# Kernel tuning notes

Hardware: AMD Instinct MI355X
Metric: run time of the kernel (lower is better)

Reference implementation:

```python
import jax, jax.numpy as jnp
import numpy as np

N = 100000      # nodes
E = 1600000     # edges (avg degree 16)
F_IN = 256      # num_features
H2 = 128        # nhid * 2 (layer 1 width)
H = 64          # nhid (layer 2 width)
C = 10          # num_classes


def setup_inputs() -> dict:
    key = jax.random.key(0)
    ks = jax.random.split(key, 8)
    x = jax.random.normal(ks[0], (N, F_IN), dtype=jnp.float32)
    edge_index = jax.random.randint(ks[1], (2, E), 0, N, dtype=jnp.int64)
    W1 = jax.random.normal(ks[2], (F_IN, H2), dtype=jnp.float32) / np.float32(np.sqrt(F_IN))
    b1 = jnp.zeros((H2,), jnp.float32)
    W2 = jax.random.normal(ks[3], (H2, H), dtype=jnp.float32) / np.float32(np.sqrt(H2))
    b2 = jnp.zeros((H,), jnp.float32)
    Wl = jax.random.normal(ks[4], (H, C), dtype=jnp.float32) / np.float32(np.sqrt(H))
    bl = jnp.zeros((C,), jnp.float32)
    return {"x": x, "edge_index": edge_index, "W1": W1, "b1": b1,
            "W2": W2, "b2": b2, "Wl": Wl, "bl": bl}


def reference(x, edge_index, W1, b1, W2, b2, Wl, bl):
    # --- GCN normalization with self-loops (PyG GCNConv default) ---
    loops = jnp.arange(N, dtype=edge_index.dtype)
    src = jnp.concatenate([edge_index[0], loops])  # message sources
    dst = jnp.concatenate([edge_index[1], loops])  # message targets
    deg = jax.ops.segment_sum(jnp.ones(src.shape[0], x.dtype), dst, num_segments=N)
    dinv = jnp.where(deg > 0, jax.lax.rsqrt(deg), 0.0)
    norm = dinv[src] * dinv[dst]                   # [E+N]

    def gcn_conv(h, W, b):
        m = h @ W                                  # transform first (out_channels small)
        agg = jax.ops.segment_sum(m[src] * norm[:, None], dst, num_segments=N)
        return agg + b

    h = jax.nn.relu(gcn_conv(x, W1, b1))           # [N, H2]
    h = jax.nn.relu(gcn_conv(h, W2, b2))           # [N, H]
    logits = h @ Wl + bl                            # [N, C]
    return jax.nn.log_softmax(logits, axis=-1)
```

## Files before the change

### kernel.cpp

```cpp
#include <hip/hip_runtime.h>


typedef unsigned short ushort_t;
typedef unsigned int uint_t;
typedef __attribute__((ext_vector_type(8))) short short8;
typedef __attribute__((ext_vector_type(4))) float floatx4;

static __device__ __forceinline__ ushort_t f2bf(float f) {
    union { float f; uint_t u; } c; c.f = f;
    return (ushort_t)((c.u + 0x8000u) >> 16);
}
static __device__ __forceinline__ float bf2f(ushort_t h) {
    union { uint_t u; float f; } c; c.u = ((uint_t)h) << 16;
    return c.f;
}
static __device__ __forceinline__ float2 up2(uint_t p) {
    union { uint_t u; float f; } lo, hi;
    lo.u = p << 16; hi.u = p & 0xffff0000u;
    return make_float2(lo.f, hi.f);
}
static __device__ __forceinline__ uint_t pk2bf(float a, float b) {
    return ((uint_t)f2bf(b) << 16) | (uint_t)f2bf(a);
}
static __device__ __forceinline__ void ld_lds16(void* lds, const void* g) {
    __builtin_amdgcn_global_load_lds(
        (const __attribute__((address_space(1))) unsigned int*)g,
        (__attribute__((address_space(3))) unsigned int*)lds, 16, 0, 0);
}

#define NBMAX 800
#define ECAP  4096

__global__ __launch_bounds__(256) void hist_kernel(
    const int* __restrict__ dst, int* __restrict__ histG,
    const float* __restrict__ W1, const float* __restrict__ W2,
    ushort_t* __restrict__ W1t, ushort_t* __restrict__ W2t,
    int* __restrict__ done, int E, int NB, int GB) {
    if ((int)blockIdx.x >= GB) {
        if ((int)blockIdx.x == GB && threadIdx.x == 0) *done = 0;
        int i = ((int)blockIdx.x - GB) * 256 + threadIdx.x;
        if (i < 256 * 128) {
            int k = i / 128, n = i % 128;
            W1t[n * 256 + k] = f2bf(W1[i]);
        }
        int j = i - 256 * 128;
        if (j >= 0 && j < 128 * 64) {
            int k = j / 64, n = j % 64;
            W2t[n * 128 + k] = f2bf(W2[j]);
        }
        return;
    }
    __shared__ int h[NBMAX];
    for (int i = threadIdx.x; i < NB; i += 256) h[i] = 0;
    __syncthreads();
    int i16 = (blockIdx.x * 256 + threadIdx.x) * 16;
    if (i16 + 15 < E) {
        #pragma unroll
        for (int u = 0; u < 4; u++) {
            int4 d = *(const int4*)(dst + i16 + u * 4);
            atomicAdd(&h[d.x >> 7], 1);
            atomicAdd(&h[d.y >> 7], 1);
            atomicAdd(&h[d.z >> 7], 1);
            atomicAdd(&h[d.w >> 7], 1);
        }
    } else {
        for (int e = i16; e < E; e++) atomicAdd(&h[dst[e] >> 7], 1);
    }
    __syncthreads();
    int* outp = histG + (size_t)blockIdx.x * NB;
    for (int i = threadIdx.x; i < NB; i += 256) outp[i] = h[i];
}

__global__ __launch_bounds__(256) void scan_bucket(
    int* __restrict__ histG, int* __restrict__ totG, int* __restrict__ bbase,
    int* __restrict__ done, int GB, int NB, int nblk) {
    __shared__ int isLast;
    __shared__ int s[256];
    int b = blockIdx.x * 256 + threadIdx.x;
    if (b < NB) {
        int run = 0;
        int g = 0;
        for (; g + 16 <= GB; g += 16) {
            int vv[16];
            #pragma unroll
            for (int u = 0; u < 16; u++) vv[u] = histG[(size_t)(g + u) * NB + b];
            #pragma unroll
            for (int u = 0; u < 16; u++) {
                histG[(size_t)(g + u) * NB + b] = run;
                run += vv[u];
            }
        }
        for (; g < GB; g++) {
            int v = histG[(size_t)g * NB + b];
            histG[(size_t)g * NB + b] = run;
            run += v;
        }
        totG[b] = run;
    }
    __threadfence();
    __syncthreads();
    if (threadIdx.x == 0)
        isLast = (atomicAdd(done, 1) == nblk - 1);
    __syncthreads();
    if (!isLast) return;
    __threadfence();
    int running = 0;
    int nch = (NB + 255) / 256;
    for (int c = 0; c < nch; c++) {
        int j = c * 256 + threadIdx.x;
        int v = (j < NB) ? totG[j] : 0;
        s[threadIdx.x] = v;
        __syncthreads();
        for (int off = 1; off < 256; off <<= 1) {
            int tmp = (threadIdx.x >= off) ? s[threadIdx.x - off] : 0;
            __syncthreads();
            s[threadIdx.x] += tmp;
            __syncthreads();
        }
        if (j < NB) bbase[j] = s[threadIdx.x] - v + running;
        int ctot = s[255];
        __syncthreads();
        running += ctot;
    }
    if (threadIdx.x == 0) bbase[NB] = running;
}

__global__ __launch_bounds__(256) void scatter_kernel(
    const int* __restrict__ src, const int* __restrict__ dst,
    const int* __restrict__ histG, const int* __restrict__ bbase,
    int* __restrict__ packed, int E, int NB) {
    __shared__ int lbase[NBMAX];
    const int* row = histG + (size_t)blockIdx.x * NB;
    for (int i = threadIdx.x; i < NB; i += 256)
        lbase[i] = bbase[i] + row[i];
    __syncthreads();
    int i16 = (blockIdx.x * 256 + threadIdx.x) * 16;
    if (i16 + 15 < E) {
        #pragma unroll
        for (int u = 0; u < 4; u++) {
            int4 s4 = *(const int4*)(src + i16 + u * 4);
            int4 d4 = *(const int4*)(dst + i16 + u * 4);
            int p;
            p = atomicAdd(&lbase[d4.x >> 7], 1); packed[p] = s4.x | ((d4.x & 127) << 17);
            p = atomicAdd(&lbase[d4.y >> 7], 1); packed[p] = s4.y | ((d4.y & 127) << 17);
            p = atomicAdd(&lbase[d4.z >> 7], 1); packed[p] = s4.z | ((d4.z & 127) << 17);
            p = atomicAdd(&lbase[d4.w >> 7], 1); packed[p] = s4.w | ((d4.w & 127) << 17);
        }
    } else {
        for (int e = i16; e < E; e++) {
            int d = dst[e];
            int p = atomicAdd(&lbase[d >> 7], 1);
            packed[p] = src[e] | ((d & 127) << 17);
        }
    }
}

__global__ __launch_bounds__(256) void bucket_csr(
    const int* __restrict__ packed, const int* __restrict__ bbase,
    int* __restrict__ rowptr, int* __restrict__ csr,
    float* __restrict__ dinv, int N, int NB) {
    __shared__ int ebuf[ECAP];
    __shared__ int cnt[128];
    __shared__ int pl[128];
    __shared__ int s[256];
    const int b = blockIdx.x;
    const int t = threadIdx.x;
    const int lo = bbase[b];
    const int hi = bbase[b + 1];
    int m = hi - lo;
    if (m > ECAP) m = ECAP;
    for (int i = t; i < m; i += 256) ebuf[i] = packed[lo + i];
    if (t < 128) cnt[t] = 0;
    __syncthreads();
    for (int i = t; i < m; i += 256) atomicAdd(&cnt[ebuf[i] >> 17], 1);
    __syncthreads();
    const int node0 = b << 7;
    int c = (t < 128) ? cnt[t] : 0;
    if (t < 128 && node0 + t < N)
        dinv[node0 + t] = rsqrtf((float)(c + 1));
    s[t] = c;
    __syncthreads();
    for (int off = 1; off < 256; off <<= 1) {
        int tmp = (t >= off) ? s[t - off] : 0;
        __syncthreads();
        s[t] += tmp;
        __syncthreads();
    }
    int excl = s[t] - c;
    if (t < 128) {
        pl[t] = excl;
        if (node0 + t <= N) rowptr[node0 + t] = lo + excl;
    }
    __syncthreads();
    for (int i = t; i < m; i += 256) {
        int e = ebuf[i];
        int p = atomicAdd(&pl[e >> 17], 1);
        csr[lo + p] = e & 0x1FFFF;
    }
}

__global__ __launch_bounds__(256) void gemm1_mfma(
    const float* __restrict__ A, const ushort_t* __restrict__ Bt,
    const float* __restrict__ dinv, ushort_t* __restrict__ out, int M) {
    __shared__ float    As[64 * 256];
    __shared__ ushort_t Bs[128 * 256];
    const int tid = threadIdx.x;
    const int l = tid & 63;
    const int wave = tid >> 6;
    const int lrow = l & 15, hh = l >> 4;
    const int m0 = blockIdx.x * 64;

    #pragma unroll
    for (int rd = 0; rd < 16; rd++) {
        int idx = rd * 256 + tid;
        int r = idx >> 6, cs = idx & 63;
        int row = m0 + r; if (row >= M) row = M - 1;
        int cl = cs ^ (r & 7);
        ld_lds16(&As[idx * 4], A + (size_t)row * 256 + cl * 4);
    }
    #pragma unroll
    for (int rd = 0; rd < 16; rd++) {
        int idx = rd * 256 + tid;
        int n = idx >> 5, cs = idx & 31;
        int cl = cs ^ (n & 7);
        ld_lds16(&Bs[idx * 8], Bt + (size_t)n * 256 + cl * 8);
    }
    __syncthreads();

    floatx4 acc[8];
    #pragma unroll
    for (int nt = 0; nt < 8; nt++)
        acc[nt] = (floatx4){0.f, 0.f, 0.f, 0.f};

    const int wr = wave * 16 + lrow;
    #pragma unroll
    for (int kk = 0; kk < 8; kk++) {
        int c0 = kk * 8 + hh * 2;
        float4 u = *(const float4*)&As[wr * 256 + ((c0    ) ^ (wr & 7)) * 4];
        float4 v = *(const float4*)&As[wr * 256 + ((c0 + 1) ^ (wr & 7)) * 4];
        short8 afr;
        afr[0] = (short)f2bf(u.x); afr[1] = (short)f2bf(u.y);
        afr[2] = (short)f2bf(u.z); afr[3] = (short)f2bf(u.w);
        afr[4] = (short)f2bf(v.x); afr[5] = (short)f2bf(v.y);
        afr[6] = (short)f2bf(v.z); afr[7] = (short)f2bf(v.w);
        short8 bfr[8];
        #pragma unroll
        for (int nt = 0; nt < 8; nt++) {
            int n = nt * 16 + lrow;
            int c = kk * 4 + hh;
            bfr[nt] = *(const short8*)&Bs[n * 256 + (c ^ (n & 7)) * 8];
        }
        #pragma unroll
        for (int nt = 0; nt < 8; nt++)
            acc[nt] = __builtin_amdgcn_mfma_f32_16x16x32_bf16(
                afr, bfr[nt], acc[nt], 0, 0, 0);
    }

    const int mbase = m0 + wave * 16 + hh * 4;
    float4 dv = *(const float4*)&dinv[mbase];
    float d[4] = {dv.x, dv.y, dv.z, dv.w};
    #pragma unroll
    for (int i = 0; i < 4; i++) {
        int m = mbase + i;
        if (m < M) {
            #pragma unroll
            for (int nt = 0; nt < 8; nt++)
                out[(size_t)m * 128 + nt * 16 + lrow] =
                    f2bf(acc[nt][i] * d[i]);
        } else if (m == M) {
            #pragma unroll
            for (int nt = 0; nt < 8; nt++)
                out[(size_t)M * 128 + nt * 16 + lrow] = 0;
        }
    }
}

__global__ __launch_bounds__(256) void gemm2_mfma(
    const ushort_t* __restrict__ A, const ushort_t* __restrict__ Bt,
    const float* __restrict__ dinv, ushort_t* __restrict__ out, int M) {
    __shared__ ushort_t As[64 * 128];
    __shared__ ushort_t Bs[64 * 128];
    const int tid = threadIdx.x;
    const int l = tid & 63;
    const int wave = tid >> 6;
    const int lrow = l & 15, hh = l >> 4;
    const int m0 = blockIdx.x * 64;

    #pragma unroll
    for (int rd = 0; rd < 4; rd++) {
        int idx = rd * 256 + tid;
        int r = idx >> 4, cs = idx & 15;
        int row = m0 + r; if (row >= M) row = M - 1;
        int cl = cs ^ (r & 7);
        ld_lds16(&As[idx * 8], A + (size_t)row * 128 + cl * 8);
    }
    #pragma unroll
    for (int rd = 0; rd < 4; rd++) {
        int idx = rd * 256 + tid;
        int n = idx >> 4, cs = idx & 15;
        int cl = cs ^ (n & 7);
        ld_lds16(&Bs[idx * 8], Bt + (size_t)n * 128 + cl * 8);
    }
    __syncthreads();

    floatx4 acc[4];
    #pragma unroll
    for (int nt = 0; nt < 4; nt++)
        acc[nt] = (floatx4){0.f, 0.f, 0.f, 0.f};

    const int wr = wave * 16 + lrow;
    #pragma unroll
    for (int kk = 0; kk < 4; kk++) {
        int c0 = kk * 4 + hh;
        short8 afr = *(const short8*)&As[wr * 128 + (c0 ^ (wr & 7)) * 8];
        short8 bfr[4];
        #pragma unroll
        for (int nt = 0; nt < 4; nt++) {
            int n = nt * 16 + lrow;
            bfr[nt] = *(const short8*)&Bs[n * 128 + (c0 ^ (n & 7)) * 8];
        }
        #pragma unroll
        for (int nt = 0; nt < 4; nt++)
            acc[nt] = __builtin_amdgcn_mfma_f32_16x16x32_bf16(
                afr, bfr[nt], acc[nt], 0, 0, 0);
    }

    const int mbase = m0 + wave * 16 + hh * 4;
    float4 dv = *(const float4*)&dinv[mbase];
    float d[4] = {dv.x, dv.y, dv.z, dv.w};
    #pragma unroll
    for (int i = 0; i < 4; i++) {
        int m = mbase + i;
        if (m < M) {
            #pragma unroll
            for (int nt = 0; nt < 4; nt++)
                out[(size_t)m * 64 + nt * 16 + lrow] =
                    f2bf(acc[nt][i] * d[i]);
        } else if (m == M) {
            #pragma unroll
            for (int nt = 0; nt < 4; nt++)
                out[(size_t)M * 64 + nt * 16 + lrow] = 0;
        }
    }
}

__global__ __launch_bounds__(256) void spmm_relu128(
    const ushort_t* __restrict__ Mm, const int* __restrict__ rowptr,
    const int* __restrict__ csr, const float* __restrict__ dinv,
    const float* __restrict__ bias, ushort_t* __restrict__ out, int n, int doff) {
    int v = (blockIdx.x * 256 + threadIdx.x) >> 6;
    int lane = threadIdx.x & 63;
    if (v >= n) return;
    int jb = rowptr[v];
    int cntn = rowptr[v + 1] - jb;
    const char* Mb = (const char*)Mm;
    const int slot = lane >> 4;
    const int q = lane & 15;
    const uint_t qb = (uint_t)q * 16;

    float2 a0 = {0.f, 0.f}, a1 = a0, a2 = a0, a3 = a0;
    if (slot == 0) {
        uint4 s = *(const uint4*)(Mb + ((size_t)v << 8) + qb);
        a0 = up2(s.x); a1 = up2(s.y); a2 = up2(s.z); a3 = up2(s.w);
    }

    for (int base = 0; base < cntn; base += 64) {
        int m = cntn - base; if (m > 64) m = 64;
        int roff = (base + lane < cntn) ? (csr[jb + base + lane] << 8) : doff;
        int m4 = (m + 3) & ~3;
        int jj = 0;
        for (; jj + 16 <= m4; jj += 16) {
            uint_t o[4];
            #pragma unroll
            for (int t = 0; t < 4; t++)
                o[t] = (uint_t)__shfl(roff, jj + 4 * t + slot) + qb;
            uint4 p[4];
            #pragma unroll
            for (int t = 0; t < 4; t++) p[t] = *(const uint4*)(Mb + o[t]);
            #pragma unroll
            for (int t = 0; t < 4; t++) {
                float2 f;
                f = up2(p[t].x); a0.x += f.x; a0.y += f.y;
                f = up2(p[t].y); a1.x += f.x; a1.y += f.y;
                f = up2(p[t].z); a2.x += f.x; a2.y += f.y;
                f = up2(p[t].w); a3.x += f.x; a3.y += f.y;
            }
        }
        for (; jj < m4; jj += 4) {
            uint_t o = (uint_t)__shfl(roff, jj + slot) + qb;
            uint4 p = *(const uint4*)(Mb + o);
            float2 f;
            f = up2(p.x); a0.x += f.x; a0.y += f.y;
            f = up2(p.y); a1.x += f.x; a1.y += f.y;
            f = up2(p.z); a2.x += f.x; a2.y += f.y;
            f = up2(p.w); a3.x += f.x; a3.y += f.y;
        }
    }
    float r[8] = {a0.x, a0.y, a1.x, a1.y, a2.x, a2.y, a3.x, a3.y};
    #pragma unroll
    for (int i = 0; i < 8; i++) r[i] += __shfl_xor(r[i], 16);
    #pragma unroll
    for (int i = 0; i < 8; i++) r[i] += __shfl_xor(r[i], 32);
    if (slot == 0) {
        float d = dinv[v];
        float4 bv0 = *(const float4*)&bias[q * 8];
        float4 bv1 = *(const float4*)&bias[q * 8 + 4];
        float o0 = fmaxf(d * r[0] + bv0.x, 0.f);
        float o1 = fmaxf(d * r[1] + bv0.y, 0.f);
        float o2 = fmaxf(d * r[2] + bv0.z, 0.f);
        float o3 = fmaxf(d * r[3] + bv0.w, 0.f);
        float o4 = fmaxf(d * r[4] + bv1.x, 0.f);
        float o5 = fmaxf(d * r[5] + bv1.y, 0.f);
        float o6 = fmaxf(d * r[6] + bv1.z, 0.f);
        float o7 = fmaxf(d * r[7] + bv1.w, 0.f);
        uint4 pk;
        pk.x = pk2bf(o0, o1); pk.y = pk2bf(o2, o3);
        pk.z = pk2bf(o4, o5); pk.w = pk2bf(o6, o7);
        *(uint4*)(out + (size_t)v * 128 + q * 8) = pk;
    }
}

__global__ __launch_bounds__(256) void spmm_relu64(
    const ushort_t* __restrict__ Mm, const int* __restrict__ rowptr,
    const int* __restrict__ csr, const float* __restrict__ dinv,
    const float* __restrict__ bias, ushort_t* __restrict__ out, int n, int doff) {
    int v = (blockIdx.x * 256 + threadIdx.x) >> 6;
    int lane = threadIdx.x & 63;
    if (v >= n) return;
    int jb = rowptr[v];
    int cntn = rowptr[v + 1] - jb;
    const char* Mb = (const char*)Mm;
    const int slot = lane >> 3;
    const int q = lane & 7;
    const uint_t qb = (uint_t)q * 16;

    float2 a0 = {0.f, 0.f}, a1 = a0, a2 = a0, a3 = a0;
    if (slot == 0) {
        uint4 s = *(const uint4*)(Mb + ((size_t)v << 7) + qb);
        a0 = up2(s.x); a1 = up2(s.y); a2 = up2(s.z); a3 = up2(s.w);
    }

    for (int base = 0; base < cntn; base += 64) {
        int m = cntn - base; if (m > 64) m = 64;
        int roff = (base + lane < cntn) ? (csr[jb + base + lane] << 7) : doff;
        int m8 = (m + 7) & ~7;
        int jj = 0;
        for (; jj + 16 <= m8; jj += 16) {
            uint_t o[2];
            #pragma unroll
            for (int t = 0; t < 2; t++)
                o[t] = (uint_t)__shfl(roff, jj + 8 * t + slot) + qb;
            uint4 p[2];
            #pragma unroll
            for (int t = 0; t < 2; t++) p[t] = *(const uint4*)(Mb + o[t]);
            #pragma unroll
            for (int t = 0; t < 2; t++) {
                float2 f;
                f = up2(p[t].x); a0.x += f.x; a0.y += f.y;
                f = up2(p[t].y); a1.x += f.x; a1.y += f.y;
                f = up2(p[t].z); a2.x += f.x; a2.y += f.y;
                f = up2(p[t].w); a3.x += f.x; a3.y += f.y;
            }
        }
        for (; jj < m8; jj += 8) {
            uint_t o = (uint_t)__shfl(roff, jj + slot) + qb;
            uint4 p = *(const uint4*)(Mb + o);
            float2 f;
            f = up2(p.x); a0.x += f.x; a0.y += f.y;
            f = up2(p.y); a1.x += f.x; a1.y += f.y;
            f = up2(p.z); a2.x += f.x; a2.y += f.y;
            f = up2(p.w); a3.x += f.x; a3.y += f.y;
        }
    }
    float r[8] = {a0.x, a0.y, a1.x, a1.y, a2.x, a2.y, a3.x, a3.y};
    #pragma unroll
    for (int i = 0; i < 8; i++) r[i] += __shfl_xor(r[i], 8);
    #pragma unroll
    for (int i = 0; i < 8; i++) r[i] += __shfl_xor(r[i], 16);
    #pragma unroll
    for (int i = 0; i < 8; i++) r[i] += __shfl_xor(r[i], 32);
    if (slot == 0) {
        float d = dinv[v];
        float4 bv0 = *(const float4*)&bias[q * 8];
        float4 bv1 = *(const float4*)&bias[q * 8 + 4];
        float o0 = fmaxf(d * r[0] + bv0.x, 0.f);
        float o1 = fmaxf(d * r[1] + bv0.y, 0.f);
        float o2 = fmaxf(d * r[2] + bv0.z, 0.f);
        float o3 = fmaxf(d * r[3] + bv0.w, 0.f);
        float o4 = fmaxf(d * r[4] + bv1.x, 0.f);
        float o5 = fmaxf(d * r[5] + bv1.y, 0.f);
        float o6 = fmaxf(d * r[6] + bv1.z, 0.f);
        float o7 = fmaxf(d * r[7] + bv1.w, 0.f);
        uint4 pk;
        pk.x = pk2bf(o0, o1); pk.y = pk2bf(o2, o3);
        pk.z = pk2bf(o4, o5); pk.w = pk2bf(o6, o7);
        *(uint4*)(out + (size_t)v * 64 + q * 8) = pk;
    }
}

__global__ __launch_bounds__(256) void head_kernel(
    const ushort_t* __restrict__ h2, const float* __restrict__ Wl,
    const float* __restrict__ bl, float* __restrict__ out, int n) {
    __shared__ float Ws[64 * 10];
    __shared__ float bs[10];
    for (int i = threadIdx.x; i < 640; i += 256) Ws[i] = Wl[i];
    if (threadIdx.x < 10) bs[threadIdx.x] = bl[threadIdx.x];
    __syncthreads();
    int v = blockIdx.x * 256 + threadIdx.x;
    if (v >= n) return;
    float acc[10];
    #pragma unroll
    for (int c = 0; c < 10; c++) acc[c] = bs[c];
    const ushort_t* hrow = &h2[(size_t)v * 64];
    #pragma unroll
    for (int k0 = 0; k0 < 64; k0 += 8) {
        short8 hv = *(const short8*)&hrow[k0];
        #pragma unroll
        for (int kk = 0; kk < 8; kk++) {
            float hf = bf2f((ushort_t)hv[kk]);
            #pragma unroll
            for (int c = 0; c < 10; c++)
                acc[c] += hf * Ws[(k0 + kk) * 10 + c];
        }
    }
    float m = acc[0];
    #pragma unroll
    for (int c = 1; c < 10; c++) m = fmaxf(m, acc[c]);
    float s = 0.f;
    #pragma unroll
    for (int c = 0; c < 10; c++) s += expf(acc[c] - m);
    float lse = logf(s);
    #pragma unroll
    for (int c = 0; c < 10; c++) out[(size_t)v * 10 + c] = acc[c] - m - lse;
}

extern "C" void kernel_launch(void* const* d_in, const int* in_sizes, int n_in,
                              void* d_out, int out_size, void* d_ws, size_t ws_size,
                              hipStream_t stream) {
    const float* x   = (const float*)d_in[0];
    const int*   ei  = (const int*)d_in[1];
    const float* W1  = (const float*)d_in[2];
    const float* b1  = (const float*)d_in[3];
    const float* W2  = (const float*)d_in[4];
    const float* b2  = (const float*)d_in[5];
    const float* Wl  = (const float*)d_in[6];
    const float* bl  = (const float*)d_in[7];
    float*       out = (float*)d_out;

    const int N = in_sizes[0] / 256;
    const int E = in_sizes[1] / 2;
    const int* srcI = ei;
    const int* dstI = ei + E;

    const int NB = (N + 127) >> 7;
    const int GB = (E + 4095) / 4096;
    const int WB = (256 * 128 + 128 * 64 + 255) / 256;
    const int SB = (NB + 255) / 256;

    char* ws = (char*)d_ws;
    size_t off = 0;
    auto alloc = [&](size_t bytes) -> void* {
        void* p = ws + off;
        off = (off + bytes + 255) & ~(size_t)255;
        return p;
    };
    int*      histG  = (int*)alloc((size_t)GB * NB * 4);
    int*      totG   = (int*)alloc((size_t)NB * 4);
    int*      bbase  = (int*)alloc((size_t)(NB + 1) * 4);
    int*      done   = (int*)alloc(256);
    int*      packed = (int*)alloc((size_t)E * 4);
    int*      rowptr = (int*)alloc((size_t)(N + 1) * 4);
    float*    dinv   = (float*)alloc((size_t)(N + 128) * 4);
    int*      csr    = (int*)alloc((size_t)E * 4);
    ushort_t* W1t    = (ushort_t*)alloc((size_t)128 * 256 * 2);
    ushort_t* W2t    = (ushort_t*)alloc((size_t)64 * 128 * 2);
    ushort_t* bufA   = (ushort_t*)alloc((size_t)(N + 2) * 128 * 2);
    ushort_t* bufB   = (ushort_t*)alloc((size_t)N * 128 * 2);

    hist_kernel<<<GB + WB, 256, 0, stream>>>(dstI, histG, W1, W2, W1t, W2t,
                                             done, E, NB, GB);
    scan_bucket<<<SB, 256, 0, stream>>>(histG, totG, bbase, done, GB, NB, SB);
    scatter_kernel<<<GB, 256, 0, stream>>>(srcI, dstI, histG, bbase, packed, E, NB);
    bucket_csr<<<NB, 256, 0, stream>>>(packed, bbase, rowptr, csr, dinv, N, NB);

    const int gblk = (N + 63) / 64;
    gemm1_mfma<<<gblk, 256, 0, stream>>>(x, W1t, dinv, bufA, N);
    spmm_relu128<<<(N + 3) / 4, 256, 0, stream>>>(bufA, rowptr, csr, dinv, b1, bufB, N, N << 8);
    gemm2_mfma<<<gblk, 256, 0, stream>>>(bufB, W2t, dinv, bufA, N);
    spmm_relu64<<<(N + 3) / 4, 256, 0, stream>>>(bufA, rowptr, csr, dinv, b2, bufB, N, N << 7);
    head_kernel<<<(N + 255) / 256, 256, 0, stream>>>(bufB, Wl, bl, out, N);
}
```

Measured before the change: 358.4 us.

## Make gemm1 persistent with double-buffered A tiles and a reloaded-once W1

The first GEMM becomes a persistent kernel with 512 blocks that loop over 32-row tiles. Each block loads W1 into LDS once and double-buffers the fp32 A tiles, so the next tile's async load overlaps the MFMA work on the current one. Waves now split the N dimension (32 columns each) rather than M, and block 0 zeroes the padding row. This aims to remove the repeated per-block W1 loads and exposed load latency, at the cost of fewer resident blocks and a larger LDS footprint per block.

```diff
diff --git a/kernel.cpp b/kernel.cpp
--- a/kernel.cpp
+++ b/kernel.cpp
@@ -201,23 +201,18 @@
 
 __global__ __launch_bounds__(256) void gemm1_mfma(
     const float* __restrict__ A, const ushort_t* __restrict__ Bt,
-    const float* __restrict__ dinv, ushort_t* __restrict__ out, int M) {
-    __shared__ float    As[64 * 256];
+    const float* __restrict__ dinv, ushort_t* __restrict__ out,
+    int M, int T) {
+    __shared__ float    As[2][32 * 256];
     __shared__ ushort_t Bs[128 * 256];
     const int tid = threadIdx.x;
     const int l = tid & 63;
     const int wave = tid >> 6;
     const int lrow = l & 15, hh = l >> 4;
-    const int m0 = blockIdx.x * 64;
-
-    #pragma unroll
-    for (int rd = 0; rd < 16; rd++) {
-        int idx = rd * 256 + tid;
-        int r = idx >> 6, cs = idx & 63;
-        int row = m0 + r; if (row >= M) row = M - 1;
-        int cl = cs ^ (r & 7);
-        ld_lds16(&As[idx * 4], A + (size_t)row * 256 + cl * 4);
-    }
+
+    if (blockIdx.x == 0 && tid < 64)
+        *(uint_t*)(out + (size_t)M * 128 + tid * 2) = 0;
+
     #pragma unroll
     for (int rd = 0; rd < 16; rd++) {
         int idx = rd * 256 + tid;
@@ -225,53 +220,87 @@
         int cl = cs ^ (n & 7);
         ld_lds16(&Bs[idx * 8], Bt + (size_t)n * 256 + cl * 8);
     }
-    __syncthreads();
-
-    floatx4 acc[8];
-    #pragma unroll
-    for (int nt = 0; nt < 8; nt++)
-        acc[nt] = (floatx4){0.f, 0.f, 0.f, 0.f};
-
-    const int wr = wave * 16 + lrow;
-    #pragma unroll
-    for (int kk = 0; kk < 8; kk++) {
-        int c0 = kk * 8 + hh * 2;
-        float4 u = *(const float4*)&As[wr * 256 + ((c0    ) ^ (wr & 7)) * 4];
-        float4 v = *(const float4*)&As[wr * 256 + ((c0 + 1) ^ (wr & 7)) * 4];
-        short8 afr;
-        afr[0] = (short)f2bf(u.x); afr[1] = (short)f2bf(u.y);
-        afr[2] = (short)f2bf(u.z); afr[3] = (short)f2bf(u.w);
-        afr[4] = (short)f2bf(v.x); afr[5] = (short)f2bf(v.y);
-        afr[6] = (short)f2bf(v.z); afr[7] = (short)f2bf(v.w);
-        short8 bfr[8];
-        #pragma unroll
-        for (int nt = 0; nt < 8; nt++) {
-            int n = nt * 16 + lrow;
-            int c = kk * 4 + hh;
-            bfr[nt] = *(const short8*)&Bs[n * 256 + (c ^ (n & 7)) * 8];
-        }
-        #pragma unroll
-        for (int nt = 0; nt < 8; nt++)
-            acc[nt] = __builtin_amdgcn_mfma_f32_16x16x32_bf16(
-                afr, bfr[nt], acc[nt], 0, 0, 0);
-    }
-
-    const int mbase = m0 + wave * 16 + hh * 4;
-    float4 dv = *(const float4*)&dinv[mbase];
-    float d[4] = {dv.x, dv.y, dv.z, dv.w};
-    #pragma unroll
-    for (int i = 0; i < 4; i++) {
-        int m = mbase + i;
-        if (m < M) {
-            #pragma unroll
-            for (int nt = 0; nt < 8; nt++)
-                out[(size_t)m * 128 + nt * 16 + lrow] =
-                    f2bf(acc[nt][i] * d[i]);
-        } else if (m == M) {
-            #pragma unroll
-            for (int nt = 0; nt < 8; nt++)
-                out[(size_t)M * 128 + nt * 16 + lrow] = 0;
-        }
+
+    auto stageA = [&](int buf, int t) {
+        int m0 = t * 32;
+        #pragma unroll
+        for (int rd = 0; rd < 8; rd++) {
+            int idx = rd * 256 + tid;
+            int r = idx >> 6, cs = idx & 63;
+            int row = m0 + r; if (row >= M) row = M - 1;
+            int cl = cs ^ (r & 7);
+            ld_lds16(&As[buf][idx * 4], A + (size_t)row * 256 + cl * 4);
+        }
+    };
+
+    const int stride = gridDim.x;
+    int t0 = blockIdx.x;
+    if (t0 >= T) return;
+    stageA(0, t0);
+    __syncthreads();
+
+    int buf = 0;
+    for (int t = t0; t < T; t += stride) {
+        int tn = t + stride;
+        if (tn < T) stageA(buf ^ 1, tn);
+
+        floatx4 acc[2][2];
+        #pragma unroll
+        for (int mt = 0; mt < 2; mt++)
+            #pragma unroll
+            for (int nt = 0; nt < 2; nt++)
+                acc[mt][nt] = (floatx4){0.f, 0.f, 0.f, 0.f};
+
+        #pragma unroll
+        for (int kk = 0; kk < 8; kk++) {
+            short8 afr[2];
+            #pragma unroll
+            for (int mt = 0; mt < 2; mt++) {
+                int r = mt * 16 + lrow;
+                int c0 = kk * 8 + hh * 2;
+                float4 u = *(const float4*)&As[buf][r * 256 + ((c0    ) ^ (r & 7)) * 4];
+                float4 v = *(const float4*)&As[buf][r * 256 + ((c0 + 1) ^ (r & 7)) * 4];
+                short8 tt;
+                tt[0] = (short)f2bf(u.x); tt[1] = (short)f2bf(u.y);
+                tt[2] = (short)f2bf(u.z); tt[3] = (short)f2bf(u.w);
+                tt[4] = (short)f2bf(v.x); tt[5] = (short)f2bf(v.y);
+                tt[6] = (short)f2bf(v.z); tt[7] = (short)f2bf(v.w);
+                afr[mt] = tt;
+            }
+            short8 bfr[2];
+            #pragma unroll
+            for (int nt = 0; nt < 2; nt++) {
+                int n = wave * 32 + nt * 16 + lrow;
+                int c = kk * 4 + hh;
+                bfr[nt] = *(const short8*)&Bs[n * 256 + (c ^ (n & 7)) * 8];
+            }
+            #pragma unroll
+            for (int mt = 0; mt < 2; mt++)
+                #pragma unroll
+                for (int nt = 0; nt < 2; nt++)
+                    acc[mt][nt] = __builtin_amdgcn_mfma_f32_16x16x32_bf16(
+                        afr[mt], bfr[nt], acc[mt][nt], 0, 0, 0);
+        }
+
+        const int m0 = t * 32;
+        #pragma unroll
+        for (int mt = 0; mt < 2; mt++) {
+            int mbase = m0 + mt * 16 + hh * 4;
+            float4 dv = *(const float4*)&dinv[mbase];
+            float d[4] = {dv.x, dv.y, dv.z, dv.w};
+            #pragma unroll
+            for (int i = 0; i < 4; i++) {
+                int m = mbase + i;
+                if (m < M) {
+                    #pragma unroll
+                    for (int nt = 0; nt < 2; nt++)
+                        out[(size_t)m * 128 + wave * 32 + nt * 16 + lrow] =
+                            f2bf(acc[mt][nt][i] * d[i]);
+                }
+            }
+        }
+        __syncthreads();
+        buf ^= 1;
     }
 }
 
@@ -583,9 +612,10 @@
     scatter_kernel<<<GB, 256, 0, stream>>>(srcI, dstI, histG, bbase, packed, E, NB);
     bucket_csr<<<NB, 256, 0, stream>>>(packed, bbase, rowptr, csr, dinv, N, NB);
 
+    const int T1 = (N + 31) / 32;
+    gemm1_mfma<<<512, 256, 0, stream>>>(x, W1t, dinv, bufA, N, T1);
+    spmm_relu128<<<(N + 3) / 4, 256, 0, stream>>>(bufA, rowptr, csr, dinv, b1, bufB, N, N << 8);
     const int gblk = (N + 63) / 64;
-    gemm1_mfma<<<gblk, 256, 0, stream>>>(x, W1t, dinv, bufA, N);
-    spmm_relu128<<<(N + 3) / 4, 256, 0, stream>>>(bufA, rowptr, csr, dinv, b1, bufB, N, N << 8);
     gemm2_mfma<<<gblk, 256, 0, stream>>>(bufB, W2t, dinv, bufA, N);
     spmm_relu64<<<(N + 3) / 4, 256, 0, stream>>>(bufA, rowptr, csr, dinv, b2, bufB, N, N << 7);
     head_kernel<<<(N + 255) / 256, 256, 0, stream>>>(bufB, Wl, bl, out, N);
```

Result: no change. 357.8 us (-0.2%).
